# Kernel optimization log

Hardware: AMD Instinct MI355X
Metric: run time of the kernel (lower is better)

The kernel has to match this reference:

```python
import jax, jax.numpy as jnp
import numpy as np

B = 512      # batch
L = 20       # reviews per user/item (L1 == L2)
N = 100      # words per review (must match between user/item, required by original bmm)
V = 50000    # vocab
D = 64       # word_dim
E = 32       # id_emb_size
U = 20000    # user_num
I = 20000    # item_num
H = 3        # point_num_heads
NT, NM = 10, 12  # travel type / month cardinalities


def _lin(x, W, b):
    # torch nn.Linear: x @ W.T + b, W is [out, in]
    return x @ W.T + b


def _hard_gumbel(logits, g):
    # F.gumbel_softmax(hard=True, tau=1, dim=1); g is pre-sampled standard Gumbel noise
    y = jax.nn.softmax(logits + g, axis=1)
    hard = jax.nn.one_hot(jnp.argmax(y, axis=1), logits.shape[1], dtype=y.dtype)
    return hard - jax.lax.stop_gradient(y) + y  # straight-through


def _coatt(u_fea, i_fea, M, Wu, bu, Wi, bi, pooling, gumbel_noise=None):
    # u_fea: [B, L1, d]; i_fea: [B, L2, d]
    u = _lin(u_fea, Wu, bu)
    i = _lin(i_fea, Wi, bi)
    S = jnp.einsum('bld,de,bme->blm', u, M, i)  # [B, L1, L2]
    if pooling == 'max':
        u_score, i_score = S.max(axis=2), S.max(axis=1)
    else:
        u_score, i_score = S.mean(axis=2), S.mean(axis=1)
    if gumbel_noise is not None:
        gu, gi = gumbel_noise
        p_u, p_i = _hard_gumbel(u_score, gu), _hard_gumbel(i_score, gi)
    else:
        p_u, p_i = jax.nn.softmax(u_score, axis=1), jax.nn.softmax(i_score, axis=1)
    return p_u[..., None], p_i[..., None]  # [B, L1, 1], [B, L2, 1]


def setup_inputs() -> dict:
    key = jax.random.key(0)
    ks = iter(jax.random.split(key, 48))
    unif = lambda shape, s=0.1: jax.random.uniform(next(ks), shape, minval=-s, maxval=s, dtype=jnp.float32)
    xav = lambda shape: jax.random.normal(next(ks), shape, dtype=jnp.float32) * np.sqrt(2.0 / (shape[-1] + shape[-2]))
    inp = {}
    inp['user_reviews'] = jax.random.randint(next(ks), (B, L, N), 0, V)
    inp['item_reviews'] = jax.random.randint(next(ks), (B, L, N), 0, V)
    inp['uids'] = jax.random.randint(next(ks), (B,), 0, U)
    inp['iids'] = jax.random.randint(next(ks), (B,), 0, I)
    inp['travel_type'] = jax.random.randint(next(ks), (B,), 0, NT)
    inp['travel_month'] = jax.random.randint(next(ks), (B,), 0, NM)
    # pre-sampled standard Gumbel noise for the hard pointer selection (one per head)
    inp['gnoise_u'] = -jnp.log(-jnp.log(jax.random.uniform(next(ks), (H, B, L), minval=1e-20, maxval=1.0)))
    inp['gnoise_i'] = -jnp.log(-jnp.log(jax.random.uniform(next(ks), (H, B, L), minval=1e-20, maxval=1.0)))
    # embedding tables
    inp['user_word_embs'] = unif((V, D))
    inp['item_word_embs'] = unif((V, D))
    inp['user_id_table'] = unif((U, E), 1.0)
    inp['item_id_table'] = unif((I, E), 1.0)
    inp['type_table'] = unif((NT, E), 1.0)
    inp['month_table'] = unif((NM, E), 1.0)
    # review gate
    inp['fc_g1_w'] = unif((D, D)); inp['fc_g1_b'] = unif((D,))
    inp['fc_g2_w'] = unif((D, D)); inp['fc_g2_b'] = unif((D,))
    # per-head co-attention params (stacked over H)
    inp['M_r'] = xav((H, D, D)); inp['Wu_r'] = unif((H, D, D)); inp['bu_r'] = unif((H, D))
    inp['Wi_r'] = unif((H, D, D)); inp['bi_r'] = unif((H, D))
    inp['M_w'] = xav((H, D, D)); inp['Wu_w'] = unif((H, D, D)); inp['bu_w'] = unif((H, D))
    inp['Wi_w'] = unif((H, D, D)); inp['bi_w'] = unif((H, D))
    inp['M_f'] = xav((H, E, E)); inp['Wu_f'] = unif((H, E, E)); inp['bu_f'] = unif((H, E))
    inp['Wi_f'] = unif((H, E, E)); inp['bi_f'] = unif((H, E))
    # projection layers
    inp['ufc_w'] = unif((E, D)); inp['ufc_b'] = unif((E,))
    inp['ifc_w'] = unif((E, D)); inp['ifc_b'] = unif((E,))
    inp['u_fc_w'] = unif((E, E * H)); inp['u_fc_b'] = unif((E,))
    inp['i_fc_w'] = unif((E, E * H)); inp['i_fc_b'] = unif((E,))
    return inp


def reference(user_reviews, item_reviews, uids, iids, travel_type, travel_month,
              gnoise_u, gnoise_i, user_word_embs, item_word_embs,
              user_id_table, item_id_table, type_table, month_table,
              fc_g1_w, fc_g1_b, fc_g2_w, fc_g2_b,
              M_r, Wu_r, bu_r, Wi_r, bi_r,
              M_w, Wu_w, bu_w, Wi_w, bi_w,
              M_f, Wu_f, bu_f, Wi_f, bi_f,
              ufc_w, ufc_b, ifc_w, ifc_b, u_fc_w, u_fc_b, i_fc_w, i_fc_b):
    # id-type embeddings -> feature stack [B, 4, E]
    user_id_emb = user_id_table[uids]
    item_id_emb = item_id_table[iids]
    type_emb = type_table[travel_type]
    month_emb = month_table[travel_month]
    feature_embedding = jnp.stack([user_id_emb, item_id_emb, type_emb, month_emb], axis=1)

    def review_gate(reviews_idx, table):
        s = table[reviews_idx].sum(axis=2)  # [B, L, N, D] -> [B, L, D]
        return jax.nn.sigmoid(_lin(s, fc_g1_w, fc_g1_b)) * jnp.tanh(_lin(s, fc_g2_w, fc_g2_b))

    u_reviews_g = review_gate(user_reviews, user_word_embs)
    i_reviews_g = review_gate(item_reviews, item_word_embs)

    u_feas, i_feas = [], []
    for h in range(H):
        # review-level pointer co-attention (hard gumbel, max pooling)
        p_u, p_i = _coatt(u_reviews_g, i_reviews_g, M_r[h], Wu_r[h], bu_r[h], Wi_r[h], bi_r[h],
                          pooling='max', gumbel_noise=(gnoise_u[h], gnoise_i[h]))
        # soft index -> cast to int (kills gradient, like torch .long()) -> word gather
        u_idx = jnp.einsum('bln,bl->bn', user_reviews.astype(p_u.dtype), p_u[..., 0]).astype(jnp.int32)
        i_idx = jnp.einsum('bln,bl->bn', item_reviews.astype(p_i.dtype), p_i[..., 0]).astype(jnp.int32)
        u_words = user_word_embs[u_idx]  # [B, N, D]
        i_words = item_word_embs[i_idx]
        # word-level co-attention (softmax, avg pooling)
        p_u2, p_i2 = _coatt(u_words, i_words, M_w[h], Wu_w[h], bu_w[h], Wi_w[h], bi_w[h], pooling='avg')
        u_w_fea = jnp.einsum('bnd,bn->bd', u_words, p_u2[..., 0])
        i_w_fea = jnp.einsum('bnd,bn->bd', u_words, p_i2[..., 0])  # NOTE: original uses u_words here (kept)
        ure = jax.nn.relu(_lin(u_w_fea, ufc_w, ufc_b))  # dropout = identity (eval)
        ire = jax.nn.relu(_lin(i_w_fea, ifc_w, ifc_b))
        review_embedding = jnp.stack([ure, ire], axis=1)  # [B, 2, E]
        review_att, fea_att = _coatt(review_embedding, feature_embedding,
                                     M_f[h], Wu_f[h], bu_f[h], Wi_f[h], bi_f[h], pooling='avg')
        fea_att_e = feature_embedding * fea_att  # [B, 4, E]
        user_id_e, item_id_e, type_e, month_e = (fea_att_e[:, 0], fea_att_e[:, 1],
                                                 fea_att_e[:, 2], fea_att_e[:, 3])
        rae = review_embedding * review_att
        user_fea_h = rae[:, 0]
        u_feas.append(user_fea_h)
        i_feas.append(user_fea_h)  # NOTE: original assigns item_fea from the user slice (kept)
    u_out = _lin(jnp.concatenate(u_feas, axis=1), u_fc_w, u_fc_b)
    i_out = _lin(jnp.concatenate(i_feas, axis=1), i_fc_w, i_fc_b)
    user_fea = jnp.stack([user_id_e, type_e, u_out], axis=1)   # [B, 3, E]
    item_fea = jnp.stack([item_id_e, month_e, i_out], axis=1)  # [B, 3, E]
    return user_fea, item_fea
```

## Files before the change

### kernel.cpp

```cpp
#include <hip/hip_runtime.h>
#include <math.h>

#define Bn 512
#define Ln 20
#define Nn 100
#define Dn 64
#define En 32
#define Hn 3

__global__ __launch_bounds__(256) void k0_all(
    const float* __restrict__ M_r, const float* __restrict__ Wu_r, const float* __restrict__ bu_r,
    const float* __restrict__ Wi_r,
    const float* __restrict__ M_w, const float* __restrict__ Wu_w, const float* __restrict__ bu_w,
    const float* __restrict__ Wi_w, const float* __restrict__ bi_w,
    const float* __restrict__ Wu_f, const float* __restrict__ Wi_f,
    const float* __restrict__ ufc, const float* __restrict__ ifc,
    const float* __restrict__ ufc2, const float* __restrict__ ifc2,
    float* __restrict__ WMr, float* __restrict__ bMr,
    float* __restrict__ GuT, float* __restrict__ GiT,
    float* __restrict__ gu_v, float* __restrict__ gi_v,
    float* __restrict__ WiT_r,
    float* __restrict__ WuT_f, float* __restrict__ WiT_f,
    float* __restrict__ ufcT, float* __restrict__ ifcT,
    float* __restrict__ u_fcT, float* __restrict__ i_fcT)
{
    __shared__ float tbuf[4][64];
    int tid = threadIdx.x, ln = tid & 63, wv = tid >> 6;
    int blk = blockIdx.x;
    if (blk < 48) {
        int W = blk*4 + wv;
        int h = W >> 6, c = W & 63;
        const float* Wu = Wu_r + h*4096;
        const float* M  = M_r  + h*4096;
        float s = 0.f;
        for (int d = 0; d < 64; ++d) s += Wu[d*64 + c] * M[d*64 + ln];
        WMr[h*4096 + c*64 + ln] = s;
    } else if (blk < 51) {
        int h = blk - 48;
        if (wv == 0) {
            float s = 0.f;
            for (int d = 0; d < 64; ++d) s += bu_r[h*64 + d] * M_r[h*4096 + d*64 + ln];
            bMr[h*64 + ln] = s;
        }
    } else if (blk < 147) {
        int W = (blk - 51)*4 + wv;
        int isGi = (W >= 192);
        int W2 = W - (isGi ? 192 : 0);
        int h = W2 >> 6, a = W2 & 63;
        float t;
        if (!isGi) {
            const float* Wu = Wu_w + h*4096; const float* M = M_w + h*4096;
            t = 0.f;
            for (int d = 0; d < 64; ++d) t += Wu[d*64 + a] * M[d*64 + ln];
        } else {
            const float* Wi = Wi_w + h*4096; const float* M = M_w + h*4096;
            t = 0.f;
            for (int d = 0; d < 64; ++d) t += M[ln*64 + d] * Wi[d*64 + a];
        }
        tbuf[wv][ln] = t;
        const float* Wsec = (isGi ? Wu_w : Wi_w) + h*4096;
        const float* bsec = (isGi ? bu_w : bi_w) + h*64;
        float s = 0.f, gvv = 0.f;
        for (int e = 0; e < 64; ++e) {
            float te = tbuf[wv][e];
            s   += te * Wsec[e*64 + ln];
            gvv += te * bsec[e];
        }
        (isGi ? GiT : GuT)[h*4096 + ln*64 + a] = s;
        if (ln == 0) (isGi ? gi_v : gu_v)[h*64 + a] = gvv;
    } else if (blk < 195) {
        int k = (blk - 147)*256 + tid;
        int h = k >> 12, r = k & 4095, c = r >> 6, dp = r & 63;
        WiT_r[k] = Wi_r[h*4096 + dp*64 + c];
    } else {
        int t = (blk - 195)*256 + tid;
        int stride = 8*256;
        for (int k = t; k < Hn*En*En; k += stride) {
            int h = k/(En*En); int rem = k - h*En*En;
            int aa = rem >> 5, c = rem & 31;
            int src = h*En*En + c*En + aa;
            WuT_f[k] = Wu_f[src]; WiT_f[k] = Wi_f[src];
        }
        for (int k = t; k < Dn*En; k += stride) {
            int d = k >> 5, e = k & 31;
            ufcT[k] = ufc[e*Dn + d]; ifcT[k] = ifc[e*Dn + d];
        }
        for (int k = t; k < 96*En; k += stride) {
            int kk = k >> 5, e = k & 31;
            u_fcT[k] = ufc2[e*96 + kk]; i_fcT[k] = ifc2[e*96 + kk];
        }
    }
}

__global__ __launch_bounds__(256) void k1_gate2(
    const int* __restrict__ urev, const int* __restrict__ irev,
    const float* __restrict__ utab, const float* __restrict__ itab,
    const float* __restrict__ W1, const float* __restrict__ b1v,
    const float* __restrict__ W2, const float* __restrict__ b2v,
    float* __restrict__ ugo, float* __restrict__ igo)
{
    __shared__ float w1s[Dn][Dn+1];
    __shared__ float w2s[Dn][Dn+1];
    __shared__ float rowb[4][Dn];
    int tid = threadIdx.x;
    for (int k = tid; k < Dn*Dn; k += 256) {
        w1s[k>>6][k&63] = W1[k];
        w2s[k>>6][k&63] = W2[k];
    }
    __syncthreads();
    int ln = tid & 63, wv = tid >> 6;
    int wid = blockIdx.x * 4 + wv;
    int r0 = ln >> 4, q4 = (ln & 15) << 2;
    float b1 = b1v[ln], b2 = b2v[ln];
    #pragma unroll 1
    for (int it = 0; it < 4; ++it) {
        int gw = wid + it * 5120;
        int side = (gw >= Bn*Ln);
        int r = gw - (side ? Bn*Ln : 0);
        const int* rev = side ? irev : urev;
        const float* tab = side ? itab : utab;
        int i0 = rev[r*Nn + ln];
        int i1 = (ln < Nn - 64) ? rev[r*Nn + 64 + ln] : 0;
        float4 buf[25];
        #pragma unroll
        for (int j = 0; j < 25; ++j) {
            int n = r0 + 4*j;
            int idx = (n < 64) ? __shfl(i0, n) : __shfl(i1, n - 64);
            buf[j] = *(const float4*)(tab + idx*Dn + q4);
        }
        float4 a = buf[0];
        #pragma unroll
        for (int j = 1; j < 25; ++j) { a.x += buf[j].x; a.y += buf[j].y; a.z += buf[j].z; a.w += buf[j].w; }
        a.x += __shfl_xor(a.x, 16); a.y += __shfl_xor(a.y, 16); a.z += __shfl_xor(a.z, 16); a.w += __shfl_xor(a.w, 16);
        a.x += __shfl_xor(a.x, 32); a.y += __shfl_xor(a.y, 32); a.z += __shfl_xor(a.z, 32); a.w += __shfl_xor(a.w, 32);
        if (ln < 16) *(float4*)(&rowb[wv][q4]) = a;
        float t1 = b1, t2 = b2;
        #pragma unroll 8
        for (int d = 0; d < Dn; ++d) {
            float sd = rowb[wv][d];
            t1 += sd * w1s[ln][d];
            t2 += sd * w2s[ln][d];
        }
        float g = (1.f / (1.f + expf(-t1))) * tanhf(t2);
        (side ? igo : ugo)[r*Dn + ln] = g;
    }
}

__global__ __launch_bounds__(256, 4) void k2_coatt(
    const int* __restrict__ urev, const int* __restrict__ irev,
    const int* __restrict__ uids, const int* __restrict__ iids,
    const int* __restrict__ ttype, const int* __restrict__ tmonth,
    const float* __restrict__ gu_all, const float* __restrict__ gi_all,
    const float* __restrict__ utab, const float* __restrict__ itab,
    const float* __restrict__ uid_tab, const float* __restrict__ iid_tab,
    const float* __restrict__ type_tab, const float* __restrict__ month_tab,
    const float* __restrict__ ug_in, const float* __restrict__ ig_in,
    const float* __restrict__ WMr, const float* __restrict__ bMr,
    const float* __restrict__ WiT_r, const float* __restrict__ bi_r,
    const float* __restrict__ GuT, const float* __restrict__ GiT,
    const float* __restrict__ gu_v, const float* __restrict__ gi_v,
    const float* __restrict__ M_f, const float* __restrict__ bu_f, const float* __restrict__ bi_f,
    const float* __restrict__ WuT_f, const float* __restrict__ WiT_f,
    const float* __restrict__ ufcT, const float* __restrict__ ufc_bv,
    const float* __restrict__ ifcT, const float* __restrict__ ifc_bv,
    float* __restrict__ feas, float* __restrict__ outp)
{
    __shared__ __align__(16) float pool[6400];
    __shared__ float vecs[4][Dn];
    __shared__ float sc[2][Nn];
    __shared__ float uif[2][Dn];
    __shared__ float att[6];
    __shared__ int   lstar[2];

    int tid = threadIdx.x;
    int bh = blockIdx.x;
    int b = bh / Hn;
    int h = bh - b*Hn;
    int ln = tid & 63;
    int wv = tid >> 6;

    {
        const float4* su = (const float4*)(ug_in + b*Ln*Dn);
        const float4* si = (const float4*)(ig_in + b*Ln*Dn);
        float4* du = (float4*)pool;
        float4* di = (float4*)(pool + 1280);
        for (int k = tid; k < (Ln*Dn)/4; k += 256) { du[k] = su[k]; di[k] = si[k]; }
    }
    __syncthreads();

    {
        int iside = wv >> 1;
        int lbase = (wv & 1) * 10;
        const float* W = (iside ? (WiT_r + h*4096) : (WMr + h*4096)) + ln;
        const float* X = pool + (iside ? 1280 : 0);
        float bias = iside ? bi_r[h*Dn + ln] : bMr[h*Dn + ln];
        float acc[10];
        #pragma unroll
        for (int l = 0; l < 10; ++l) acc[l] = 0.f;
        for (int dd = 0; dd < Dn; dd += 4) {
            float w0 = W[(dd+0)*Dn];
            float w1 = W[(dd+1)*Dn];
            float w2 = W[(dd+2)*Dn];
            float w3 = W[(dd+3)*Dn];
            #pragma unroll
            for (int l = 0; l < 10; ++l) {
                float4 x = *(const float4*)(X + (lbase+l)*Dn + dd);
                acc[l] += x.x*w0 + x.y*w1 + x.z*w2 + x.w*w3;
            }
        }
        float* out = pool + (iside ? 3840 : 2560);
        #pragma unroll
        for (int l = 0; l < 10; ++l) {
            int lg = lbase + l;
            out[lg*Dn + (ln ^ lg)] = acc[l] + bias;
        }
    }
    __syncthreads();
    for (int k = tid; k < Ln*Ln; k += 256) {
        int l = k / Ln, m = k - l*Ln;
        const float* Ab = pool + 2560 + l*Dn;
        const float* iv = pool + 3840 + m*Dn;
        float a = 0.f;
        for (int e = 0; e < Dn; ++e) a += Ab[e ^ l] * iv[e ^ m];
        pool[5120 + k] = a;
    }
    __syncthreads();
    if (wv == 0) {
        float v = -3.4e38f;
        if (ln < Ln) {
            float mx = pool[5120 + ln*Ln];
            #pragma unroll
            for (int m = 1; m < Ln; ++m) mx = fmaxf(mx, pool[5120 + ln*Ln + m]);
            v = mx + gu_all[(h*Bn + b)*Ln + ln];
        }
        int idx = ln;
        #pragma unroll
        for (int off = 32; off > 0; off >>= 1) {
            float ov = __shfl_down(v, off);
            int oi = __shfl_down(idx, off);
            if (ov > v || (ov == v && oi < idx)) { v = ov; idx = oi; }
        }
        if (ln == 0) lstar[0] = idx;
    } else if (wv == 1) {
        float v = -3.4e38f;
        if (ln < Ln) {
            float mx = pool[5120 + ln];
            #pragma unroll
            for (int l = 1; l < Ln; ++l) mx = fmaxf(mx, pool[5120 + l*Ln + ln]);
            v = mx + gi_all[(h*Bn + b)*Ln + ln];
        }
        int idx = ln;
        #pragma unroll
        for (int off = 32; off > 0; off >>= 1) {
            float ov = __shfl_down(v, off);
            int oi = __shfl_down(idx, off);
            if (ov > v || (ov == v && oi < idx)) { v = ov; idx = oi; }
        }
        if (ln == 0) lstar[1] = idx;
    }
    __syncthreads();

    int rubase = (b*Ln + lstar[0])*Nn;
    int ribase = (b*Ln + lstar[1])*Nn;
    int r0 = ln >> 4;
    int q4 = (ln & 15) << 2;
    int idxr[25];

    if (wv < 2) {
        for (int k = tid; k < Nn*16; k += 128) {
            int n = k >> 4, qi = k & 15;
            int idx = urev[rubase + n];
            float4 v = *(const float4*)(utab + idx*Dn + (qi << 2));
            *(float4*)(pool + n*Dn + (((qi ^ (n & 15)) << 2))) = v;
        }
    } else {
        const int* rev = (wv == 2) ? irev : urev;
        const float* tab = (wv == 2) ? itab : utab;
        int rb = (wv == 2) ? ribase : rubase;
        #pragma unroll
        for (int j = 0; j < 25; ++j) idxr[j] = rev[rb + r0 + 4*j];
        float4 s = make_float4(0.f, 0.f, 0.f, 0.f);
        #pragma unroll 5
        for (int g = 0; g < 5; ++g) {
            float4 v0 = *(const float4*)(tab + idxr[g*5+0]*Dn + q4);
            float4 v1 = *(const float4*)(tab + idxr[g*5+1]*Dn + q4);
            float4 v2 = *(const float4*)(tab + idxr[g*5+2]*Dn + q4);
            float4 v3 = *(const float4*)(tab + idxr[g*5+3]*Dn + q4);
            float4 v4 = *(const float4*)(tab + idxr[g*5+4]*Dn + q4);
            s.x += v0.x+v1.x+v2.x+v3.x+v4.x;
            s.y += v0.y+v1.y+v2.y+v3.y+v4.y;
            s.z += v0.z+v1.z+v2.z+v3.z+v4.z;
            s.w += v0.w+v1.w+v2.w+v3.w+v4.w;
        }
        s.x += __shfl_xor(s.x, 16); s.y += __shfl_xor(s.y, 16); s.z += __shfl_xor(s.z, 16); s.w += __shfl_xor(s.w, 16);
        s.x += __shfl_xor(s.x, 32); s.y += __shfl_xor(s.y, 32); s.z += __shfl_xor(s.z, 32); s.w += __shfl_xor(s.w, 32);
        if (ln < 16) {
            float4 m = make_float4(s.x*(1.f/Nn), s.y*(1.f/Nn), s.z*(1.f/Nn), s.w*(1.f/Nn));
            *(float4*)(&vecs[(wv == 2) ? 1 : 0][q4]) = m;
        }
    }
    __syncthreads();

    if (tid < Dn) {
        float a = gu_v[h*Dn + tid];
        for (int bb = 0; bb < Dn; ++bb) a += GuT[h*4096 + bb*Dn + tid] * vecs[1][bb];
        vecs[2][tid] = a;
    } else if (tid < 2*Dn) {
        int aa = tid - Dn;
        float a = gi_v[h*Dn + aa];
        for (int bb = 0; bb < Dn; ++bb) a += GiT[h*4096 + bb*Dn + aa] * vecs[0][bb];
        vecs[3][aa] = a;
    }
    __syncthreads();

    if (tid < Nn) {
        float a = 0.f;
        const float* row = pool + tid*Dn;
        int sw = tid & 15;
        #pragma unroll
        for (int qi = 0; qi < 16; ++qi) {
            float4 w = *(const float4*)(&vecs[2][qi << 2]);
            float4 x = *(const float4*)(row + ((qi ^ sw) << 2));
            a += x.x*w.x + x.y*w.y + x.z*w.z + x.w*w.w;
        }
        sc[0][tid] = a;
    } else if (wv == 2) {
        float4 wq = *(const float4*)(&vecs[3][q4]);
        #pragma unroll 5
        for (int g = 0; g < 5; ++g) {
            float p0, p1, p2, p3, p4;
            {
                float4 v0 = *(const float4*)(itab + idxr[g*5+0]*Dn + q4);
                float4 v1 = *(const float4*)(itab + idxr[g*5+1]*Dn + q4);
                float4 v2 = *(const float4*)(itab + idxr[g*5+2]*Dn + q4);
                float4 v3 = *(const float4*)(itab + idxr[g*5+3]*Dn + q4);
                float4 v4 = *(const float4*)(itab + idxr[g*5+4]*Dn + q4);
                p0 = v0.x*wq.x + v0.y*wq.y + v0.z*wq.z + v0.w*wq.w;
                p1 = v1.x*wq.x + v1.y*wq.y + v1.z*wq.z + v1.w*wq.w;
                p2 = v2.x*wq.x + v2.y*wq.y + v2.z*wq.z + v2.w*wq.w;
                p3 = v3.x*wq.x + v3.y*wq.y + v3.z*wq.z + v3.w*wq.w;
                p4 = v4.x*wq.x + v4.y*wq.y + v4.z*wq.z + v4.w*wq.w;
            }
            #pragma unroll
            for (int off = 1; off < 16; off <<= 1) {
                p0 += __shfl_xor(p0, off); p1 += __shfl_xor(p1, off);
                p2 += __shfl_xor(p2, off); p3 += __shfl_xor(p3, off);
                p4 += __shfl_xor(p4, off);
            }
            if ((ln & 15) == 0) {
                sc[1][r0 + 4*(g*5+0)] = p0;
                sc[1][r0 + 4*(g*5+1)] = p1;
                sc[1][r0 + 4*(g*5+2)] = p2;
                sc[1][r0 + 4*(g*5+3)] = p3;
                sc[1][r0 + 4*(g*5+4)] = p4;
            }
        }
    }
    __syncthreads();
    if (wv == 0 || wv == 2) {
        float* s = sc[wv >> 1];
        float x0 = s[ln];
        float x1 = (ln < Nn - 64) ? s[64 + ln] : -3.4e38f;
        float mx = fmaxf(x0, x1);
        #pragma unroll
        for (int off = 32; off > 0; off >>= 1) mx = fmaxf(mx, __shfl_xor(mx, off));
        float e0 = expf(x0 - mx);
        float e1 = (ln < Nn - 64) ? expf(x1 - mx) : 0.f;
        float sum = e0 + e1;
        #pragma unroll
        for (int off = 32; off > 0; off >>= 1) sum += __shfl_xor(sum, off);
        float inv = 1.f / sum;
        s[ln] = e0 * inv;
        if (ln < Nn - 64) s[64 + ln] = e1 * inv;
    }
    __syncthreads();
    if (tid < 2*Dn) {
        int which = tid >> 6;
        int d = tid & 63;
        int qt = (d >> 2), dl = d & 3;
        const float* p = sc[which];
        float a = 0.f;
        for (int n = 0; n < Nn; ++n)
            a += p[n] * pool[n*Dn + ((qt ^ (n & 15)) << 2) + dl];
        uif[which][d] = a;
    }
    __syncthreads();
    float* fe_ = pool;
    float* re_ = pool + 128;
    float* u3_ = pool + 192;
    float* i3_ = pool + 256;
    float* A3_ = pool + 384;
    if (tid < En) {
        float a = ufc_bv[tid];
        for (int d = 0; d < Dn; ++d) a += uif[0][d] * ufcT[d*En + tid];
        re_[tid] = fmaxf(a, 0.f);
    } else if (tid < 2*En) {
        int e = tid - En;
        float a = ifc_bv[e];
        for (int d = 0; d < Dn; ++d) a += uif[1][d] * ifcT[d*En + e];
        re_[En + e] = fmaxf(a, 0.f);
    } else if (tid < 2*En + 4*En) {
        int j = tid - 2*En;
        int rrow = j >> 5, e = j & 31;
        float v;
        if (rrow == 0) v = uid_tab[uids[b]*En + e];
        else if (rrow == 1) v = iid_tab[iids[b]*En + e];
        else if (rrow == 2) v = type_tab[ttype[b]*En + e];
        else v = month_tab[tmonth[b]*En + e];
        fe_[j] = v;
    }
    __syncthreads();
    const float* WuTf = WuT_f + h*En*En;
    const float* WiTf = WiT_f + h*En*En;
    const float* Mf   = M_f  + h*En*En;
    if (tid < 2*En) {
        int l = tid >> 5, e = tid & 31;
        float a = bu_f[h*En + e];
        for (int j = 0; j < En; ++j) a += re_[l*En + j] * WuTf[j*En + e];
        u3_[tid] = a;
    } else if (tid < 6*En) {
        int t2 = tid - 2*En;
        int m = t2 >> 5, e = t2 & 31;
        float a = bi_f[h*En + e];
        for (int j = 0; j < En; ++j) a += fe_[m*En + j] * WiTf[j*En + e];
        i3_[t2] = a;
    }
    __syncthreads();
    if (tid < 2*En) {
        int l = tid >> 5, e = tid & 31;
        float a = 0.f;
        for (int d = 0; d < En; ++d) a += u3_[l*En + d] * Mf[d*En + e];
        A3_[tid] = a;
    }
    __syncthreads();
    if (tid == 0) {
        float S3[2][4];
        for (int l = 0; l < 2; ++l)
            for (int m = 0; m < 4; ++m) {
                float a = 0.f;
                for (int e = 0; e < En; ++e) a += A3_[l*En + e] * i3_[m*En + e];
                S3[l][m] = a;
            }
        float us0 = (S3[0][0] + S3[0][1] + S3[0][2] + S3[0][3]) * 0.25f;
        float us1 = (S3[1][0] + S3[1][1] + S3[1][2] + S3[1][3]) * 0.25f;
        float mx = fmaxf(us0, us1);
        float e0 = expf(us0 - mx), e1 = expf(us1 - mx);
        float inv = 1.f / (e0 + e1);
        att[0] = e0 * inv; att[1] = e1 * inv;
        float is_[4]; float mxi = -3.4e38f;
        for (int m = 0; m < 4; ++m) { is_[m] = (S3[0][m] + S3[1][m]) * 0.5f; mxi = fmaxf(mxi, is_[m]); }
        float ssum = 0.f, ee[4];
        for (int m = 0; m < 4; ++m) { ee[m] = expf(is_[m] - mxi); ssum += ee[m]; }
        float invi = 1.f / ssum;
        for (int m = 0; m < 4; ++m) att[2 + m] = ee[m] * invi;
    }
    __syncthreads();
    if (tid < En) {
        feas[b*96 + h*En + tid] = re_[tid] * att[0];
    }
    if (h == 2) {
        if (tid >= 32 && tid < 64)        { int e = tid - 32;  outp[b*96 + e]              = fe_[e]      * att[2]; }
        else if (tid >= 64 && tid < 96)   { int e = tid - 64;  outp[b*96 + 32 + e]         = fe_[64 + e] * att[4]; }
        else if (tid >= 96 && tid < 128)  { int e = tid - 96;  outp[Bn*96 + b*96 + e]      = fe_[32 + e] * att[3]; }
        else if (tid >= 128 && tid < 160) { int e = tid - 128; outp[Bn*96 + b*96 + 32 + e] = fe_[96 + e] * att[5]; }
    }
}

__global__ __launch_bounds__(64) void k3_final(
    const float* __restrict__ feas,
    const float* __restrict__ u_fcT, const float* __restrict__ u_fc_bv,
    const float* __restrict__ i_fcT, const float* __restrict__ i_fc_bv,
    float* __restrict__ outp)
{
    __shared__ float f[96];
    int b = blockIdx.x, tid = threadIdx.x;
    for (int k = tid; k < 96; k += 64) f[k] = feas[b*96 + k];
    __syncthreads();
    if (tid < 32) {
        float a = u_fc_bv[tid];
        for (int k = 0; k < 96; ++k) a += f[k] * u_fcT[k*32 + tid];
        outp[b*96 + 64 + tid] = a;
    } else {
        int e = tid - 32;
        float a = i_fc_bv[e];
        for (int k = 0; k < 96; ++k) a += f[k] * i_fcT[k*32 + e];
        outp[Bn*96 + b*96 + 64 + e] = a;
    }
}

extern "C" void kernel_launch(void* const* d_in, const int* in_sizes, int n_in,
                              void* d_out, int out_size, void* d_ws, size_t ws_size,
                              hipStream_t stream)
{
    const int* urev = (const int*)d_in[0];
    const int* irev = (const int*)d_in[1];
    const int* uids = (const int*)d_in[2];
    const int* iids = (const int*)d_in[3];
    const int* ttype = (const int*)d_in[4];
    const int* tmonth = (const int*)d_in[5];
    const float* gu = (const float*)d_in[6];
    const float* gi = (const float*)d_in[7];
    const float* utab = (const float*)d_in[8];
    const float* itab = (const float*)d_in[9];
    const float* uid_tab = (const float*)d_in[10];
    const float* iid_tab = (const float*)d_in[11];
    const float* type_tab = (const float*)d_in[12];
    const float* month_tab = (const float*)d_in[13];
    const float* fc_g1_w = (const float*)d_in[14];
    const float* fc_g1_b = (const float*)d_in[15];
    const float* fc_g2_w = (const float*)d_in[16];
    const float* fc_g2_b = (const float*)d_in[17];
    const float* M_r = (const float*)d_in[18];
    const float* Wu_r = (const float*)d_in[19];
    const float* bu_r = (const float*)d_in[20];
    const float* Wi_r = (const float*)d_in[21];
    const float* bi_r = (const float*)d_in[22];
    const float* M_w = (const float*)d_in[23];
    const float* Wu_w = (const float*)d_in[24];
    const float* bu_w = (const float*)d_in[25];
    const float* Wi_w = (const float*)d_in[26];
    const float* bi_w = (const float*)d_in[27];
    const float* M_f = (const float*)d_in[28];
    const float* Wu_f = (const float*)d_in[29];
    const float* bu_f = (const float*)d_in[30];
    const float* Wi_f = (const float*)d_in[31];
    const float* bi_f = (const float*)d_in[32];
    const float* ufc_w = (const float*)d_in[33];
    const float* ufc_b = (const float*)d_in[34];
    const float* ifc_w = (const float*)d_in[35];
    const float* ifc_b = (const float*)d_in[36];
    const float* u_fc_w = (const float*)d_in[37];
    const float* u_fc_b = (const float*)d_in[38];
    const float* i_fc_w = (const float*)d_in[39];
    const float* i_fc_b = (const float*)d_in[40];
    (void)in_sizes; (void)n_in; (void)out_size; (void)ws_size;

    float* ws = (float*)d_ws;
    float* ugo   = ws;
    float* igo   = ugo + Bn*Ln*Dn;
    float* feas  = igo + Bn*Ln*Dn;
    float* WiT_r = feas + Bn*96;
    float* WMr   = WiT_r + Hn*Dn*Dn;
    float* bMr   = WMr + Hn*Dn*Dn;
    float* GuT   = bMr + Hn*Dn;
    float* GiT   = GuT + Hn*Dn*Dn;
    float* gu_v  = GiT + Hn*Dn*Dn;
    float* gi_v  = gu_v + Hn*Dn;
    float* WuT_f = gi_v + Hn*Dn;
    float* WiT_f = WuT_f + Hn*En*En;
    float* ufcT  = WiT_f + Hn*En*En;
    float* ifcT  = ufcT + Dn*En;
    float* u_fcT = ifcT + Dn*En;
    float* i_fcT = u_fcT + 96*En;

    hipLaunchKernelGGL(k0_all, dim3(203), dim3(256), 0, stream,
        M_r, Wu_r, bu_r, Wi_r, M_w, Wu_w, bu_w, Wi_w, bi_w,
        Wu_f, Wi_f, ufc_w, ifc_w, u_fc_w, i_fc_w,
        WMr, bMr, GuT, GiT, gu_v, gi_v, WiT_r,
        WuT_f, WiT_f, ufcT, ifcT, u_fcT, i_fcT);

    hipLaunchKernelGGL(k1_gate2, dim3(1280), dim3(256), 0, stream,
        urev, irev, utab, itab, fc_g1_w, fc_g1_b, fc_g2_w, fc_g2_b, ugo, igo);

    hipLaunchKernelGGL(k2_coatt, dim3(Bn*Hn), dim3(256), 0, stream,
        urev, irev, uids, iids, ttype, tmonth, gu, gi, utab, itab,
        uid_tab, iid_tab, type_tab, month_tab, ugo, igo,
        WMr, bMr, WiT_r, bi_r, GuT, GiT, gu_v, gi_v,
        M_f, bu_f, bi_f, WuT_f, WiT_f,
        ufcT, ufc_b, ifcT, ifc_b, feas, (float*)d_out);

    hipLaunchKernelGGL(k3_final, dim3(Bn), dim3(64), 0, stream,
        feas, u_fcT, u_fc_b, i_fcT, i_fc_b, (float*)d_out);
}
```

Baseline: 292.6 us.

## Fuse coattention and final FC into one kernel with one wavefront per head

The per-(batch,head) coattention kernel and the final FC kernel are merged into one kernel launched once per batch row. Each of three wavefronts handles one head end to end with its own shared-memory slab, so most block-wide barriers disappear, and a fourth wave gathers the feature embeddings. The aim is to drop a launch and the global round trip through the feas buffer, and to load the gated inputs once per batch instead of once per head. In exchange each head now runs on a single wave instead of four, the grid is a third of its former size, and register pressure rises with the 20-row accumulators.

```diff
diff --git a/kernel.cpp b/kernel.cpp
--- a/kernel.cpp
+++ b/kernel.cpp
@@ -7,6 +7,19 @@
 #define Dn 64
 #define En 32
 #define Hn 3
+
+#define AB_  0
+#define IV_  1280
+#define SS_  2560
+#define SC_  2960
+#define VB_  3160
+#define UIF_ 3416
+#define RE_  3544
+#define U3_  3608
+#define I3_  3672
+#define A3_  3800
+#define ATT_ 3864
+#define SLABN 3872
 
 __global__ __launch_bounds__(256) void k0_all(
     const float* __restrict__ M_r, const float* __restrict__ Wu_r, const float* __restrict__ bu_r,
@@ -146,7 +159,7 @@
     }
 }
 
-__global__ __launch_bounds__(256, 4) void k2_coatt(
+__global__ __launch_bounds__(256, 2) void k2_fused(
     const int* __restrict__ urev, const int* __restrict__ irev,
     const int* __restrict__ uids, const int* __restrict__ iids,
     const int* __restrict__ ttype, const int* __restrict__ tmonth,
@@ -163,328 +176,277 @@
     const float* __restrict__ WuT_f, const float* __restrict__ WiT_f,
     const float* __restrict__ ufcT, const float* __restrict__ ufc_bv,
     const float* __restrict__ ifcT, const float* __restrict__ ifc_bv,
-    float* __restrict__ feas, float* __restrict__ outp)
-{
-    __shared__ __align__(16) float pool[6400];
-    __shared__ float vecs[4][Dn];
-    __shared__ float sc[2][Nn];
-    __shared__ float uif[2][Dn];
-    __shared__ float att[6];
-    __shared__ int   lstar[2];
-
-    int tid = threadIdx.x;
-    int bh = blockIdx.x;
-    int b = bh / Hn;
-    int h = bh - b*Hn;
-    int ln = tid & 63;
-    int wv = tid >> 6;
-
-    {
-        const float4* su = (const float4*)(ug_in + b*Ln*Dn);
-        const float4* si = (const float4*)(ig_in + b*Ln*Dn);
-        float4* du = (float4*)pool;
-        float4* di = (float4*)(pool + 1280);
-        for (int k = tid; k < (Ln*Dn)/4; k += 256) { du[k] = su[k]; di[k] = si[k]; }
-    }
-    __syncthreads();
-
-    {
-        int iside = wv >> 1;
-        int lbase = (wv & 1) * 10;
-        const float* W = (iside ? (WiT_r + h*4096) : (WMr + h*4096)) + ln;
-        const float* X = pool + (iside ? 1280 : 0);
-        float bias = iside ? bi_r[h*Dn + ln] : bMr[h*Dn + ln];
-        float acc[10];
-        #pragma unroll
-        for (int l = 0; l < 10; ++l) acc[l] = 0.f;
-        for (int dd = 0; dd < Dn; dd += 4) {
-            float w0 = W[(dd+0)*Dn];
-            float w1 = W[(dd+1)*Dn];
-            float w2 = W[(dd+2)*Dn];
-            float w3 = W[(dd+3)*Dn];
-            #pragma unroll
-            for (int l = 0; l < 10; ++l) {
-                float4 x = *(const float4*)(X + (lbase+l)*Dn + dd);
-                acc[l] += x.x*w0 + x.y*w1 + x.z*w2 + x.w*w3;
-            }
-        }
-        float* out = pool + (iside ? 3840 : 2560);
-        #pragma unroll
-        for (int l = 0; l < 10; ++l) {
-            int lg = lbase + l;
-            out[lg*Dn + (ln ^ lg)] = acc[l] + bias;
-        }
-    }
-    __syncthreads();
-    for (int k = tid; k < Ln*Ln; k += 256) {
-        int l = k / Ln, m = k - l*Ln;
-        const float* Ab = pool + 2560 + l*Dn;
-        const float* iv = pool + 3840 + m*Dn;
-        float a = 0.f;
-        for (int e = 0; e < Dn; ++e) a += Ab[e ^ l] * iv[e ^ m];
-        pool[5120 + k] = a;
-    }
-    __syncthreads();
-    if (wv == 0) {
-        float v = -3.4e38f;
-        if (ln < Ln) {
-            float mx = pool[5120 + ln*Ln];
-            #pragma unroll
-            for (int m = 1; m < Ln; ++m) mx = fmaxf(mx, pool[5120 + ln*Ln + m]);
-            v = mx + gu_all[(h*Bn + b)*Ln + ln];
-        }
-        int idx = ln;
-        #pragma unroll
-        for (int off = 32; off > 0; off >>= 1) {
-            float ov = __shfl_down(v, off);
-            int oi = __shfl_down(idx, off);
-            if (ov > v || (ov == v && oi < idx)) { v = ov; idx = oi; }
-        }
-        if (ln == 0) lstar[0] = idx;
-    } else if (wv == 1) {
-        float v = -3.4e38f;
-        if (ln < Ln) {
-            float mx = pool[5120 + ln];
-            #pragma unroll
-            for (int l = 1; l < Ln; ++l) mx = fmaxf(mx, pool[5120 + l*Ln + ln]);
-            v = mx + gi_all[(h*Bn + b)*Ln + ln];
-        }
-        int idx = ln;
-        #pragma unroll
-        for (int off = 32; off > 0; off >>= 1) {
-            float ov = __shfl_down(v, off);
-            int oi = __shfl_down(idx, off);
-            if (ov > v || (ov == v && oi < idx)) { v = ov; idx = oi; }
-        }
-        if (ln == 0) lstar[1] = idx;
-    }
-    __syncthreads();
-
-    int rubase = (b*Ln + lstar[0])*Nn;
-    int ribase = (b*Ln + lstar[1])*Nn;
-    int r0 = ln >> 4;
-    int q4 = (ln & 15) << 2;
-    int idxr[25];
-
-    if (wv < 2) {
-        for (int k = tid; k < Nn*16; k += 128) {
-            int n = k >> 4, qi = k & 15;
-            int idx = urev[rubase + n];
-            float4 v = *(const float4*)(utab + idx*Dn + (qi << 2));
-            *(float4*)(pool + n*Dn + (((qi ^ (n & 15)) << 2))) = v;
-        }
-    } else {
-        const int* rev = (wv == 2) ? irev : urev;
-        const float* tab = (wv == 2) ? itab : utab;
-        int rb = (wv == 2) ? ribase : rubase;
-        #pragma unroll
-        for (int j = 0; j < 25; ++j) idxr[j] = rev[rb + r0 + 4*j];
-        float4 s = make_float4(0.f, 0.f, 0.f, 0.f);
-        #pragma unroll 5
-        for (int g = 0; g < 5; ++g) {
-            float4 v0 = *(const float4*)(tab + idxr[g*5+0]*Dn + q4);
-            float4 v1 = *(const float4*)(tab + idxr[g*5+1]*Dn + q4);
-            float4 v2 = *(const float4*)(tab + idxr[g*5+2]*Dn + q4);
-            float4 v3 = *(const float4*)(tab + idxr[g*5+3]*Dn + q4);
-            float4 v4 = *(const float4*)(tab + idxr[g*5+4]*Dn + q4);
-            s.x += v0.x+v1.x+v2.x+v3.x+v4.x;
-            s.y += v0.y+v1.y+v2.y+v3.y+v4.y;
-            s.z += v0.z+v1.z+v2.z+v3.z+v4.z;
-            s.w += v0.w+v1.w+v2.w+v3.w+v4.w;
-        }
-        s.x += __shfl_xor(s.x, 16); s.y += __shfl_xor(s.y, 16); s.z += __shfl_xor(s.z, 16); s.w += __shfl_xor(s.w, 16);
-        s.x += __shfl_xor(s.x, 32); s.y += __shfl_xor(s.y, 32); s.z += __shfl_xor(s.z, 32); s.w += __shfl_xor(s.w, 32);
-        if (ln < 16) {
-            float4 m = make_float4(s.x*(1.f/Nn), s.y*(1.f/Nn), s.z*(1.f/Nn), s.w*(1.f/Nn));
-            *(float4*)(&vecs[(wv == 2) ? 1 : 0][q4]) = m;
-        }
-    }
-    __syncthreads();
-
-    if (tid < Dn) {
-        float a = gu_v[h*Dn + tid];
-        for (int bb = 0; bb < Dn; ++bb) a += GuT[h*4096 + bb*Dn + tid] * vecs[1][bb];
-        vecs[2][tid] = a;
-    } else if (tid < 2*Dn) {
-        int aa = tid - Dn;
-        float a = gi_v[h*Dn + aa];
-        for (int bb = 0; bb < Dn; ++bb) a += GiT[h*4096 + bb*Dn + aa] * vecs[0][bb];
-        vecs[3][aa] = a;
-    }
-    __syncthreads();
-
-    if (tid < Nn) {
-        float a = 0.f;
-        const float* row = pool + tid*Dn;
-        int sw = tid & 15;
-        #pragma unroll
-        for (int qi = 0; qi < 16; ++qi) {
-            float4 w = *(const float4*)(&vecs[2][qi << 2]);
-            float4 x = *(const float4*)(row + ((qi ^ sw) << 2));
-            a += x.x*w.x + x.y*w.y + x.z*w.z + x.w*w.w;
-        }
-        sc[0][tid] = a;
-    } else if (wv == 2) {
-        float4 wq = *(const float4*)(&vecs[3][q4]);
-        #pragma unroll 5
-        for (int g = 0; g < 5; ++g) {
-            float p0, p1, p2, p3, p4;
-            {
-                float4 v0 = *(const float4*)(itab + idxr[g*5+0]*Dn + q4);
-                float4 v1 = *(const float4*)(itab + idxr[g*5+1]*Dn + q4);
-                float4 v2 = *(const float4*)(itab + idxr[g*5+2]*Dn + q4);
-                float4 v3 = *(const float4*)(itab + idxr[g*5+3]*Dn + q4);
-                float4 v4 = *(const float4*)(itab + idxr[g*5+4]*Dn + q4);
-                p0 = v0.x*wq.x + v0.y*wq.y + v0.z*wq.z + v0.w*wq.w;
-                p1 = v1.x*wq.x + v1.y*wq.y + v1.z*wq.z + v1.w*wq.w;
-                p2 = v2.x*wq.x + v2.y*wq.y + v2.z*wq.z + v2.w*wq.w;
-                p3 = v3.x*wq.x + v3.y*wq.y + v3.z*wq.z + v3.w*wq.w;
-                p4 = v4.x*wq.x + v4.y*wq.y + v4.z*wq.z + v4.w*wq.w;
-            }
-            #pragma unroll
-            for (int off = 1; off < 16; off <<= 1) {
-                p0 += __shfl_xor(p0, off); p1 += __shfl_xor(p1, off);
-                p2 += __shfl_xor(p2, off); p3 += __shfl_xor(p3, off);
-                p4 += __shfl_xor(p4, off);
-            }
-            if ((ln & 15) == 0) {
-                sc[1][r0 + 4*(g*5+0)] = p0;
-                sc[1][r0 + 4*(g*5+1)] = p1;
-                sc[1][r0 + 4*(g*5+2)] = p2;
-                sc[1][r0 + 4*(g*5+3)] = p3;
-                sc[1][r0 + 4*(g*5+4)] = p4;
-            }
-        }
-    }
-    __syncthreads();
-    if (wv == 0 || wv == 2) {
-        float* s = sc[wv >> 1];
-        float x0 = s[ln];
-        float x1 = (ln < Nn - 64) ? s[64 + ln] : -3.4e38f;
-        float mx = fmaxf(x0, x1);
-        #pragma unroll
-        for (int off = 32; off > 0; off >>= 1) mx = fmaxf(mx, __shfl_xor(mx, off));
-        float e0 = expf(x0 - mx);
-        float e1 = (ln < Nn - 64) ? expf(x1 - mx) : 0.f;
-        float sum = e0 + e1;
-        #pragma unroll
-        for (int off = 32; off > 0; off >>= 1) sum += __shfl_xor(sum, off);
-        float inv = 1.f / sum;
-        s[ln] = e0 * inv;
-        if (ln < Nn - 64) s[64 + ln] = e1 * inv;
-    }
-    __syncthreads();
-    if (tid < 2*Dn) {
-        int which = tid >> 6;
-        int d = tid & 63;
-        int qt = (d >> 2), dl = d & 3;
-        const float* p = sc[which];
-        float a = 0.f;
-        for (int n = 0; n < Nn; ++n)
-            a += p[n] * pool[n*Dn + ((qt ^ (n & 15)) << 2) + dl];
-        uif[which][d] = a;
-    }
-    __syncthreads();
-    float* fe_ = pool;
-    float* re_ = pool + 128;
-    float* u3_ = pool + 192;
-    float* i3_ = pool + 256;
-    float* A3_ = pool + 384;
-    if (tid < En) {
-        float a = ufc_bv[tid];
-        for (int d = 0; d < Dn; ++d) a += uif[0][d] * ufcT[d*En + tid];
-        re_[tid] = fmaxf(a, 0.f);
-    } else if (tid < 2*En) {
-        int e = tid - En;
-        float a = ifc_bv[e];
-        for (int d = 0; d < Dn; ++d) a += uif[1][d] * ifcT[d*En + e];
-        re_[En + e] = fmaxf(a, 0.f);
-    } else if (tid < 2*En + 4*En) {
-        int j = tid - 2*En;
-        int rrow = j >> 5, e = j & 31;
-        float v;
-        if (rrow == 0) v = uid_tab[uids[b]*En + e];
-        else if (rrow == 1) v = iid_tab[iids[b]*En + e];
-        else if (rrow == 2) v = type_tab[ttype[b]*En + e];
-        else v = month_tab[tmonth[b]*En + e];
-        fe_[j] = v;
-    }
-    __syncthreads();
-    const float* WuTf = WuT_f + h*En*En;
-    const float* WiTf = WiT_f + h*En*En;
-    const float* Mf   = M_f  + h*En*En;
-    if (tid < 2*En) {
-        int l = tid >> 5, e = tid & 31;
-        float a = bu_f[h*En + e];
-        for (int j = 0; j < En; ++j) a += re_[l*En + j] * WuTf[j*En + e];
-        u3_[tid] = a;
-    } else if (tid < 6*En) {
-        int t2 = tid - 2*En;
-        int m = t2 >> 5, e = t2 & 31;
-        float a = bi_f[h*En + e];
-        for (int j = 0; j < En; ++j) a += fe_[m*En + j] * WiTf[j*En + e];
-        i3_[t2] = a;
-    }
-    __syncthreads();
-    if (tid < 2*En) {
-        int l = tid >> 5, e = tid & 31;
-        float a = 0.f;
-        for (int d = 0; d < En; ++d) a += u3_[l*En + d] * Mf[d*En + e];
-        A3_[tid] = a;
-    }
-    __syncthreads();
-    if (tid == 0) {
-        float S3[2][4];
-        for (int l = 0; l < 2; ++l)
-            for (int m = 0; m < 4; ++m) {
-                float a = 0.f;
-                for (int e = 0; e < En; ++e) a += A3_[l*En + e] * i3_[m*En + e];
-                S3[l][m] = a;
-            }
-        float us0 = (S3[0][0] + S3[0][1] + S3[0][2] + S3[0][3]) * 0.25f;
-        float us1 = (S3[1][0] + S3[1][1] + S3[1][2] + S3[1][3]) * 0.25f;
-        float mx = fmaxf(us0, us1);
-        float e0 = expf(us0 - mx), e1 = expf(us1 - mx);
-        float inv = 1.f / (e0 + e1);
-        att[0] = e0 * inv; att[1] = e1 * inv;
-        float is_[4]; float mxi = -3.4e38f;
-        for (int m = 0; m < 4; ++m) { is_[m] = (S3[0][m] + S3[1][m]) * 0.5f; mxi = fmaxf(mxi, is_[m]); }
-        float ssum = 0.f, ee[4];
-        for (int m = 0; m < 4; ++m) { ee[m] = expf(is_[m] - mxi); ssum += ee[m]; }
-        float invi = 1.f / ssum;
-        for (int m = 0; m < 4; ++m) att[2 + m] = ee[m] * invi;
-    }
-    __syncthreads();
-    if (tid < En) {
-        feas[b*96 + h*En + tid] = re_[tid] * att[0];
-    }
-    if (h == 2) {
-        if (tid >= 32 && tid < 64)        { int e = tid - 32;  outp[b*96 + e]              = fe_[e]      * att[2]; }
-        else if (tid >= 64 && tid < 96)   { int e = tid - 64;  outp[b*96 + 32 + e]         = fe_[64 + e] * att[4]; }
-        else if (tid >= 96 && tid < 128)  { int e = tid - 96;  outp[Bn*96 + b*96 + e]      = fe_[32 + e] * att[3]; }
-        else if (tid >= 128 && tid < 160) { int e = tid - 128; outp[Bn*96 + b*96 + 32 + e] = fe_[96 + e] * att[5]; }
-    }
-}
-
-__global__ __launch_bounds__(64) void k3_final(
-    const float* __restrict__ feas,
     const float* __restrict__ u_fcT, const float* __restrict__ u_fc_bv,
     const float* __restrict__ i_fcT, const float* __restrict__ i_fc_bv,
     float* __restrict__ outp)
 {
-    __shared__ float f[96];
-    int b = blockIdx.x, tid = threadIdx.x;
-    for (int k = tid; k < 96; k += 64) f[k] = feas[b*96 + k];
+    __shared__ __align__(16) float ug_s[Ln*Dn];
+    __shared__ __align__(16) float ig_s[Ln*Dn];
+    __shared__ float fe_s[4*En];
+    __shared__ float fin[96];
+    __shared__ __align__(16) float slab[3][SLABN];
+
+    int tid = threadIdx.x;
+    int b = blockIdx.x;
+    int ln = tid & 63;
+    int wv = tid >> 6;
+
+    {
+        const float4* su = (const float4*)(ug_in + b*Ln*Dn);
+        const float4* si = (const float4*)(ig_in + b*Ln*Dn);
+        for (int k = tid; k < (Ln*Dn)/4; k += 256) {
+            ((float4*)ug_s)[k] = su[k];
+            ((float4*)ig_s)[k] = si[k];
+        }
+    }
+    if (wv == 3) {
+        for (int k = ln; k < 4*En; k += 64) {
+            int rrow = k >> 5, e = k & 31;
+            float v;
+            if (rrow == 0) v = uid_tab[uids[b]*En + e];
+            else if (rrow == 1) v = iid_tab[iids[b]*En + e];
+            else if (rrow == 2) v = type_tab[ttype[b]*En + e];
+            else v = month_tab[tmonth[b]*En + e];
+            fe_s[k] = v;
+        }
+    }
     __syncthreads();
-    if (tid < 32) {
-        float a = u_fc_bv[tid];
-        for (int k = 0; k < 96; ++k) a += f[k] * u_fcT[k*32 + tid];
-        outp[b*96 + 64 + tid] = a;
-    } else {
-        int e = tid - 32;
-        float a = i_fc_bv[e];
-        for (int k = 0; k < 96; ++k) a += f[k] * i_fcT[k*32 + e];
-        outp[Bn*96 + b*96 + 64 + e] = a;
+
+    if (wv < 3) {
+        int h = wv;
+        float* sl = slab[wv];
+        int r0 = ln >> 4;
+        int q4 = (ln & 15) << 2;
+
+        {
+            float ab[Ln], iv[Ln];
+            #pragma unroll
+            for (int l = 0; l < Ln; ++l) { ab[l] = 0.f; iv[l] = 0.f; }
+            const float* Wm = WMr + h*4096 + ln;
+            const float* Wi = WiT_r + h*4096 + ln;
+            for (int d0 = 0; d0 < Dn; d0 += 4) {
+                float w0 = Wm[(d0+0)*64], w1 = Wm[(d0+1)*64], w2 = Wm[(d0+2)*64], w3 = Wm[(d0+3)*64];
+                float v0 = Wi[(d0+0)*64], v1 = Wi[(d0+1)*64], v2 = Wi[(d0+2)*64], v3 = Wi[(d0+3)*64];
+                #pragma unroll
+                for (int l = 0; l < Ln; ++l) {
+                    float4 xu = *(const float4*)(ug_s + l*Dn + d0);
+                    float4 xi = *(const float4*)(ig_s + l*Dn + d0);
+                    ab[l] += xu.x*w0 + xu.y*w1 + xu.z*w2 + xu.w*w3;
+                    iv[l] += xi.x*v0 + xi.y*v1 + xi.z*v2 + xi.w*v3;
+                }
+            }
+            float bA = bMr[h*64 + ln], bI = bi_r[h*64 + ln];
+            #pragma unroll
+            for (int l = 0; l < Ln; ++l) {
+                sl[AB_ + l*64 + (ln ^ l)] = ab[l] + bA;
+                sl[IV_ + l*64 + (ln ^ l)] = iv[l] + bI;
+            }
+        }
+        for (int k = ln; k < Ln*Ln; k += 64) {
+            int l = k / Ln, m = k - l*Ln;
+            float a = 0.f;
+            for (int e = 0; e < Dn; ++e)
+                a += sl[AB_ + l*64 + (e ^ l)] * sl[IV_ + m*64 + (e ^ m)];
+            sl[SS_ + k] = a;
+        }
+        int lu, li;
+        {
+            float v = -3.4e38f;
+            if (ln < Ln) {
+                float mx = sl[SS_ + ln*Ln];
+                #pragma unroll
+                for (int m = 1; m < Ln; ++m) mx = fmaxf(mx, sl[SS_ + ln*Ln + m]);
+                v = mx + gu_all[(h*Bn + b)*Ln + ln];
+            }
+            int idx = ln;
+            #pragma unroll
+            for (int off = 32; off > 0; off >>= 1) {
+                float ov = __shfl_down(v, off);
+                int oi = __shfl_down(idx, off);
+                if (ov > v || (ov == v && oi < idx)) { v = ov; idx = oi; }
+            }
+            lu = __shfl(idx, 0);
+        }
+        {
+            float v = -3.4e38f;
+            if (ln < Ln) {
+                float mx = sl[SS_ + ln];
+                #pragma unroll
+                for (int l = 1; l < Ln; ++l) mx = fmaxf(mx, sl[SS_ + l*Ln + ln]);
+                v = mx + gi_all[(h*Bn + b)*Ln + ln];
+            }
+            int idx = ln;
+            #pragma unroll
+            for (int off = 32; off > 0; off >>= 1) {
+                float ov = __shfl_down(v, off);
+                int oi = __shfl_down(idx, off);
+                if (ov > v || (ov == v && oi < idx)) { v = ov; idx = oi; }
+            }
+            li = __shfl(idx, 0);
+        }
+        int rub = (b*Ln + lu)*Nn;
+        int rib = (b*Ln + li)*Nn;
+        int idxu[25], idxi[25];
+        #pragma unroll
+        for (int j = 0; j < 25; ++j) {
+            idxu[j] = urev[rub + r0 + 4*j];
+            idxi[j] = irev[rib + r0 + 4*j];
+        }
+        #pragma unroll
+        for (int sd = 0; sd < 2; ++sd) {
+            const float* tab = sd ? itab : utab;
+            const int* ix = sd ? idxi : idxu;
+            float4 s = make_float4(0.f, 0.f, 0.f, 0.f);
+            #pragma unroll 5
+            for (int g = 0; g < 5; ++g) {
+                float4 v0 = *(const float4*)(tab + ix[g*5+0]*Dn + q4);
+                float4 v1 = *(const float4*)(tab + ix[g*5+1]*Dn + q4);
+                float4 v2 = *(const float4*)(tab + ix[g*5+2]*Dn + q4);
+                float4 v3 = *(const float4*)(tab + ix[g*5+3]*Dn + q4);
+                float4 v4 = *(const float4*)(tab + ix[g*5+4]*Dn + q4);
+                s.x += v0.x+v1.x+v2.x+v3.x+v4.x;
+                s.y += v0.y+v1.y+v2.y+v3.y+v4.y;
+                s.z += v0.z+v1.z+v2.z+v3.z+v4.z;
+                s.w += v0.w+v1.w+v2.w+v3.w+v4.w;
+            }
+            s.x += __shfl_xor(s.x, 16); s.y += __shfl_xor(s.y, 16); s.z += __shfl_xor(s.z, 16); s.w += __shfl_xor(s.w, 16);
+            s.x += __shfl_xor(s.x, 32); s.y += __shfl_xor(s.y, 32); s.z += __shfl_xor(s.z, 32); s.w += __shfl_xor(s.w, 32);
+            if (ln < 16) {
+                float4 m = make_float4(s.x*(1.f/Nn), s.y*(1.f/Nn), s.z*(1.f/Nn), s.w*(1.f/Nn));
+                *(float4*)(&sl[VB_ + sd*64 + q4]) = m;
+            }
+        }
+        {
+            float a1 = gu_v[h*64 + ln], a2 = gi_v[h*64 + ln];
+            for (int bb = 0; bb < 64; ++bb) {
+                a1 += GuT[h*4096 + bb*64 + ln] * sl[VB_ + 64 + bb];
+                a2 += GiT[h*4096 + bb*64 + ln] * sl[VB_ + bb];
+            }
+            sl[VB_ + 128 + ln] = a1;
+            sl[VB_ + 192 + ln] = a2;
+        }
+        #pragma unroll
+        for (int sd = 0; sd < 2; ++sd) {
+            const float* tab = sd ? itab : utab;
+            const int* ix = sd ? idxi : idxu;
+            float4 wq = *(const float4*)(&sl[VB_ + 128 + sd*64 + q4]);
+            #pragma unroll 5
+            for (int j = 0; j < 25; ++j) {
+                float4 v = *(const float4*)(tab + ix[j]*Dn + q4);
+                float p = v.x*wq.x + v.y*wq.y + v.z*wq.z + v.w*wq.w;
+                #pragma unroll
+                for (int off = 1; off < 16; off <<= 1) p += __shfl_xor(p, off);
+                if ((ln & 15) == 0) sl[SC_ + sd*100 + r0 + 4*j] = p;
+            }
+        }
+        #pragma unroll
+        for (int sd = 0; sd < 2; ++sd) {
+            float* s = &sl[SC_ + sd*100];
+            float x0 = s[ln];
+            float x1 = (ln < Nn - 64) ? s[64 + ln] : -3.4e38f;
+            float mx = fmaxf(x0, x1);
+            #pragma unroll
+            for (int off = 32; off > 0; off >>= 1) mx = fmaxf(mx, __shfl_xor(mx, off));
+            float e0 = expf(x0 - mx);
+            float e1 = (ln < Nn - 64) ? expf(x1 - mx) : 0.f;
+            float sum = e0 + e1;
+            #pragma unroll
+            for (int off = 32; off > 0; off >>= 1) sum += __shfl_xor(sum, off);
+            float inv = 1.f / sum;
+            s[ln] = e0 * inv;
+            if (ln < Nn - 64) s[64 + ln] = e1 * inv;
+        }
+        {
+            float4 au = make_float4(0.f,0.f,0.f,0.f), ai = make_float4(0.f,0.f,0.f,0.f);
+            #pragma unroll 5
+            for (int j = 0; j < 25; ++j) {
+                int n = r0 + 4*j;
+                float4 v = *(const float4*)(utab + idxu[j]*Dn + q4);
+                float pu = sl[SC_ + n];
+                float pi = sl[SC_ + 100 + n];
+                au.x += pu*v.x; au.y += pu*v.y; au.z += pu*v.z; au.w += pu*v.w;
+                ai.x += pi*v.x; ai.y += pi*v.y; ai.z += pi*v.z; ai.w += pi*v.w;
+            }
+            au.x += __shfl_xor(au.x,16); au.y += __shfl_xor(au.y,16); au.z += __shfl_xor(au.z,16); au.w += __shfl_xor(au.w,16);
+            au.x += __shfl_xor(au.x,32); au.y += __shfl_xor(au.y,32); au.z += __shfl_xor(au.z,32); au.w += __shfl_xor(au.w,32);
+            ai.x += __shfl_xor(ai.x,16); ai.y += __shfl_xor(ai.y,16); ai.z += __shfl_xor(ai.z,16); ai.w += __shfl_xor(ai.w,16);
+            ai.x += __shfl_xor(ai.x,32); ai.y += __shfl_xor(ai.y,32); ai.z += __shfl_xor(ai.z,32); ai.w += __shfl_xor(ai.w,32);
+            if (ln < 16) {
+                *(float4*)(&sl[UIF_ + q4]) = au;
+                *(float4*)(&sl[UIF_ + 64 + q4]) = ai;
+            }
+        }
+        {
+            int e = ln & 31;
+            int sd = ln >> 5;
+            const float* T = sd ? ifcT : ufcT;
+            float a = (sd ? ifc_bv : ufc_bv)[e];
+            for (int d = 0; d < Dn; ++d) a += sl[UIF_ + sd*64 + d] * T[d*En + e];
+            sl[RE_ + ln] = fmaxf(a, 0.f);
+        }
+        const float* WuTf = WuT_f + h*En*En;
+        const float* WiTf = WiT_f + h*En*En;
+        const float* Mf   = M_f  + h*En*En;
+        {
+            int l = ln >> 5, e = ln & 31;
+            float a = bu_f[h*En + e];
+            for (int j = 0; j < En; ++j) a += sl[RE_ + l*En + j] * WuTf[j*En + e];
+            sl[U3_ + ln] = a;
+            #pragma unroll
+            for (int mm = 0; mm < 2; ++mm) {
+                int m = mm*2 + l;
+                float c = bi_f[h*En + e];
+                for (int j = 0; j < En; ++j) c += fe_s[m*En + j] * WiTf[j*En + e];
+                sl[I3_ + m*En + e] = c;
+            }
+            float a3 = 0.f;
+            for (int d = 0; d < En; ++d) a3 += sl[U3_ + l*En + d] * Mf[d*En + e];
+            sl[A3_ + ln] = a3;
+        }
+        if (ln < 8) {
+            int l = ln >> 2, m = ln & 3;
+            float a = 0.f;
+            for (int e = 0; e < En; ++e) a += sl[A3_ + l*En + e] * sl[I3_ + m*En + e];
+            sl[SS_ + ln] = a;
+        }
+        if (ln == 0) {
+            float S3[2][4];
+            for (int l = 0; l < 2; ++l)
+                for (int m = 0; m < 4; ++m) S3[l][m] = sl[SS_ + l*4 + m];
+            float us0 = (S3[0][0]+S3[0][1]+S3[0][2]+S3[0][3]) * 0.25f;
+            float us1 = (S3[1][0]+S3[1][1]+S3[1][2]+S3[1][3]) * 0.25f;
+            float mx = fmaxf(us0, us1);
+            float e0 = expf(us0 - mx), e1 = expf(us1 - mx);
+            float inv = 1.f / (e0 + e1);
+            sl[ATT_ + 0] = e0 * inv; sl[ATT_ + 1] = e1 * inv;
+            float is_[4]; float mxi = -3.4e38f;
+            for (int m = 0; m < 4; ++m) { is_[m] = (S3[0][m] + S3[1][m]) * 0.5f; mxi = fmaxf(mxi, is_[m]); }
+            float ssum = 0.f, ee[4];
+            for (int m = 0; m < 4; ++m) { ee[m] = expf(is_[m] - mxi); ssum += ee[m]; }
+            float invi = 1.f / ssum;
+            for (int m = 0; m < 4; ++m) sl[ATT_ + 2 + m] = ee[m] * invi;
+        }
+        if (ln < En) {
+            fin[wv*En + ln] = sl[RE_ + ln] * sl[ATT_ + 0];
+        }
+        if (h == 2) {
+            for (int k = ln; k < 128; k += 64) {
+                int rrow = k >> 5, e = k & 31;
+                float v = fe_s[rrow*En + e] * sl[ATT_ + 2 + rrow];
+                if (rrow == 0)      outp[b*96 + e] = v;
+                else if (rrow == 1) outp[Bn*96 + b*96 + e] = v;
+                else if (rrow == 2) outp[b*96 + 32 + e] = v;
+                else                outp[Bn*96 + b*96 + 32 + e] = v;
+            }
+        }
+    }
+    __syncthreads();
+    if (tid < 64) {
+        int e = tid & 31, sd = tid >> 5;
+        const float* T = sd ? i_fcT : u_fcT;
+        float a = (sd ? i_fc_bv : u_fc_bv)[e];
+        for (int k = 0; k < 96; ++k) a += fin[k] * T[k*32 + e];
+        outp[(sd ? Bn*96 : 0) + b*96 + 64 + e] = a;
     }
 }
 
@@ -538,8 +500,7 @@
     float* ws = (float*)d_ws;
     float* ugo   = ws;
     float* igo   = ugo + Bn*Ln*Dn;
-    float* feas  = igo + Bn*Ln*Dn;
-    float* WiT_r = feas + Bn*96;
+    float* WiT_r = igo + Bn*Ln*Dn;
     float* WMr   = WiT_r + Hn*Dn*Dn;
     float* bMr   = WMr + Hn*Dn*Dn;
     float* GuT   = bMr + Hn*Dn;
@@ -562,13 +523,11 @@
     hipLaunchKernelGGL(k1_gate2, dim3(1280), dim3(256), 0, stream,
         urev, irev, utab, itab, fc_g1_w, fc_g1_b, fc_g2_w, fc_g2_b, ugo, igo);
 
-    hipLaunchKernelGGL(k2_coatt, dim3(Bn*Hn), dim3(256), 0, stream,
+    hipLaunchKernelGGL(k2_fused, dim3(Bn), dim3(256), 0, stream,
         urev, irev, uids, iids, ttype, tmonth, gu, gi, utab, itab,
         uid_tab, iid_tab, type_tab, month_tab, ugo, igo,
         WMr, bMr, WiT_r, bi_r, GuT, GiT, gu_v, gi_v,
         M_f, bu_f, bi_f, WuT_f, WiT_f,
-        ufcT, ufc_b, ifcT, ifc_b, feas, (float*)d_out);
-
-    hipLaunchKernelGGL(k3_final, dim3(Bn), dim3(64), 0, stream,
-        feas, u_fcT, u_fc_b, i_fcT, i_fc_b, (float*)d_out);
+        ufcT, ufc_b, ifcT, ifc_b, u_fcT, u_fc_b, i_fcT, i_fc_b,
+        (float*)d_out);
 }
```

Measured after the change: 289.3 us. About the same (-1.1%).
